# Kernel optimization log

Measured on AMD Instinct MI355X. Metric: run time of the kernel, lower is better.

The kernel has to match this reference:

```python
import jax, jax.numpy as jnp
jax.config.update("jax_enable_x64", True)
import numpy as np

B_, H_, W_, O_ = 8, 96, 96, 8
STRIDES = 1


def generate_px_coordinates(shape, coord_K, strides=1):
    # coord_K: [B,2,2]; row 0 = per-axis scale, row 1 = per-axis offset
    H, W = shape
    u = jnp.arange(W, dtype=coord_K.dtype)[None, None, :]
    v = jnp.arange(H, dtype=coord_K.dtype)[None, :, None]
    u = u * strides * coord_K[:, 0, 0][:, None, None] + coord_K[:, 1, 0][:, None, None]
    v = v * strides * coord_K[:, 0, 1][:, None, None] + coord_K[:, 1, 1][:, None, None]
    B = coord_K.shape[0]
    return jnp.broadcast_to(u, (B, H, W)), jnp.broadcast_to(v, (B, H, W))


def matrix_A(obj, TCR):
    # obj: [B,H,W,O,3]; TCR: [B,4,4] -> A: [B,H,W,O,4,13]
    p1 = obj[..., 0:1]
    p2 = obj[..., 1:2]
    p3 = obj[..., 2:3]
    one = jnp.ones_like(p1)
    T1 = TCR[:, None, None, None, :, 0]
    T2 = TCR[:, None, None, None, :, 1]
    T3 = TCR[:, None, None, None, :, 2]
    T4 = TCR[:, None, None, None, :, 3]
    return jnp.stack((p1 * T1, p2 * T1, p3 * T1,
                      p1 * T2, p2 * T2, p3 * T2,
                      p1 * T3, p2 * T3, p3 * T3,
                      one * T4, one * T1, one * T2, one * T3), axis=-1)


def matrix_B(shape, camera_matrix, coord_K, strides=1):
    # -> [B,H,W,2,4]
    u, v = generate_px_coordinates(shape, coord_K, strides)
    coords = jnp.stack([u, v], axis=-1)[..., None]  # [B,H,W,2,1]
    left4 = -jnp.eye(2, dtype=camera_matrix.dtype)[None, None, None] \
            * camera_matrix[:, None, None, :2, :2]  # [B,H,W,2,2]
    Bn, H, W = u.shape
    left4 = jnp.broadcast_to(left4, (Bn, H, W, 2, 2))
    d1_2 = coords - camera_matrix[:, None, None, :2, 2:3]  # [B,H,W,2,1]
    return jnp.concatenate([left4, d1_2, jnp.zeros_like(d1_2)], axis=-1)


def setup_inputs() -> dict:
    key = jax.random.key(0)
    k1, k2, k3, k4 = jax.random.split(key, 4)
    obj = jax.random.normal(k1, (B_, H_, W_, O_, 3), dtype=jnp.float32)
    w_pixel = jax.random.normal(k2, (B_, H_, W_, O_, 4), dtype=jnp.float32)
    camera_matrix = jax.random.normal(k3, (B_, 3, 3), dtype=jnp.float32)
    coord_K = jax.random.uniform(k4, (B_, 2, 2), dtype=jnp.float32)
    return {"obj": obj, "w_pixel": w_pixel,
            "camera_matrix": camera_matrix, "coord_K": coord_K}


def reference(obj, w_pixel, camera_matrix, coord_K):
    B, H, W, O = obj.shape[:4]
    Wp = w_pixel.reshape(B, H, W, O, 2, 2)
    TCR = jnp.broadcast_to(jnp.eye(4, dtype=obj.dtype), (B, 4, 4))
    A = matrix_A(obj, TCR)                                  # [B,H,W,O,4,13]
    Bm = matrix_B((H, W), camera_matrix, coord_K, STRIDES)  # [B,H,W,2,4]
    BA = jnp.einsum('bxyij,bxyojk->bxyoik', Bm, A)          # [B,H,W,O,2,13]
    MRow = jnp.matmul(Wp, BA)                               # [B,H,W,O,2,13]
    num_eq = 2 * H * W
    M = jnp.transpose(MRow, (0, 3, 1, 2, 4, 5)).reshape(B, O, num_eq, 13)
    M = M.astype(jnp.float64)
    return jnp.matmul(jnp.swapaxes(M, -1, -2), M)           # [B,O,13,13]
```

## Files before the change

### kernel.cpp

```cpp
#include <hip/hip_runtime.h>

#define B_ 8
#define H_ 96
#define W_ 96
#define O_ 8
#define HW_ (H_ * W_)
#define NT 512
#define NPART ((NT / 64) * 8)

__global__ __launch_bounds__(NT) void mtm_kernel(
    const float* __restrict__ obj,
    const float* __restrict__ wpx,
    const float* __restrict__ cam,
    const float* __restrict__ ck,
    float* __restrict__ out)
{
    const int bo = blockIdx.x;
    const int b  = bo >> 3;
    const int o  = bo & 7;

    const float* cm = cam + b * 9;
    const float* k4 = ck  + b * 4;
    const float a   = -cm[0];
    const float c   = -cm[4];
    const float k00 = k4[0];
    const float k01 = k4[1];
    const float Bu  = k4[2] - cm[2];
    const float Bv  = k4[3] - cm[5];

    float acc[60];
#pragma unroll
    for (int s = 0; s < 60; ++s) acc[s] = 0.f;

    const int baseo = (b * HW_) * O_ + o;

    for (int p = threadIdx.x; p < HW_; p += NT) {
        const int h = p / W_;
        const int w = p - h * W_;
        const int slot = baseo + p * O_;

        const float* ob = obj + slot * 3;
        const float p1 = ob[0], p2 = ob[1], p3 = ob[2];
        const float4 wp = *(const float4*)(wpx + slot * 4);

        const float du = fmaf((float)w, k00, Bu);
        const float dv = fmaf((float)h, k01, Bv);

        const float x00 = wp.x * a;
        const float x01 = wp.y * c;
        const float x02 = fmaf(wp.x, du, wp.y * dv);
        const float x10 = wp.z * a;
        const float x11 = wp.w * c;
        const float x12 = fmaf(wp.z, du, wp.w * dv);

        float Xa[6];
        Xa[0] = fmaf(x00, x00, x10 * x10);
        Xa[1] = fmaf(x00, x01, x10 * x11);
        Xa[2] = fmaf(x00, x02, x10 * x12);
        Xa[3] = fmaf(x01, x01, x11 * x11);
        Xa[4] = fmaf(x01, x02, x11 * x12);
        Xa[5] = fmaf(x02, x02, x12 * x12);

        float Q[10];
        Q[0] = p1 * p1; Q[1] = p1 * p2; Q[2] = p1 * p3; Q[3] = p1;
        Q[4] = p2 * p2; Q[5] = p2 * p3; Q[6] = p2;
        Q[7] = p3 * p3; Q[8] = p3;
        Q[9] = 1.f;

#pragma unroll
        for (int ij = 0; ij < 6; ++ij) {
#pragma unroll
            for (int kl = 0; kl < 10; ++kl)
                acc[ij * 10 + kl] = fmaf(Xa[ij], Q[kl], acc[ij * 10 + kl]);
        }
    }

#pragma unroll
    for (int s = 0; s < 60; ++s) {
        float v = acc[s];
        v += __shfl_xor(v, 8,  64);
        v += __shfl_xor(v, 16, 64);
        v += __shfl_xor(v, 32, 64);
        acc[s] = v;
    }

    __shared__ float lds[NPART * 60];
    __shared__ float S[60];
    const int lane = threadIdx.x & 63;
    const int wave = threadIdx.x >> 6;
    if (lane < 8) {
#pragma unroll
        for (int s = 0; s < 60; ++s)
            lds[(wave * 8 + lane) * 60 + s] = acc[s];
    }
    __syncthreads();

    if (threadIdx.x < 60) {
        float v = 0.f;
#pragma unroll
        for (int t = 0; t < NPART; ++t) v += lds[t * 60 + threadIdx.x];
        S[threadIdx.x] = v;
    }
    __syncthreads();

    for (int t = threadIdx.x; t < 169; t += NT) {
        const int r = t / 13;
        const int cc = t - r * 13;
        float val = 0.f;
        if (r != 9 && cc != 9) {
            int i, k, j, l;
            if (r < 9)  { i = r / 3;  k = r - i * 3; } else { i = r - 10;  k = 3; }
            if (cc < 9) { j = cc / 3; l = cc - j * 3; } else { j = cc - 10; l = 3; }
            const int ii = i < j ? i : j, jj = i < j ? j : i;
            const int kk = k < l ? k : l, ll = k < l ? l : k;
            const int ijIdx = ii * (5 - ii) / 2 + jj;
            const int klIdx = kk * (7 - kk) / 2 + ll;
            val = S[ijIdx * 10 + klIdx];
        }
        out[bo * 169 + t] = val;
    }
}

extern "C" void kernel_launch(void* const* d_in, const int* in_sizes, int n_in,
                              void* d_out, int out_size, void* d_ws, size_t ws_size,
                              hipStream_t stream) {
    const float* obj = (const float*)d_in[0];
    const float* wpx = (const float*)d_in[1];
    const float* cam = (const float*)d_in[2];
    const float* ck  = (const float*)d_in[3];
    float* out = (float*)d_out;

    mtm_kernel<<<dim3(B_ * O_), dim3(NT), 0, stream>>>(obj, wpx, cam, ck, out);
}
```

Baseline: 91.07 us.

## Split pixel range across many blocks per batch and reduce via atomics

The grid changes from 64 blocks (one per batch/object pair) to 72 chunks per batch, 576 blocks in all. Within a block, threads map to (object, pixel) so global loads of obj and w_pixel are contiguous. Partial 13x13 results are combined into the output with float atomicAdd after a memset, which aims to fill the GPU instead of leaving most CUs idle. The cost is an extra memset, many atomic adds, and a summation order that now varies from run to run.

Measured after the change: 84.18 us. 7.6% less time.

```diff
diff --git a/kernel.cpp b/kernel.cpp
--- a/kernel.cpp
+++ b/kernel.cpp
@@ -6,7 +6,9 @@
 #define O_ 8
 #define HW_ (H_ * W_)
 #define NT 512
-#define NPART ((NT / 64) * 8)
+#define NCH 72
+#define PPB (HW_ / NCH)
+#define ITERS (PPB / 64)
 
 __global__ __launch_bounds__(NT) void mtm_kernel(
     const float* __restrict__ obj,
@@ -15,9 +17,8 @@
     const float* __restrict__ ck,
     float* __restrict__ out)
 {
-    const int bo = blockIdx.x;
-    const int b  = bo >> 3;
-    const int o  = bo & 7;
+    const int chunk = blockIdx.x;
+    const int b     = blockIdx.y;
 
     const float* cm = cam + b * 9;
     const float* k4 = ck  + b * 4;
@@ -28,20 +29,23 @@
     const float Bu  = k4[2] - cm[2];
     const float Bv  = k4[3] - cm[5];
 
+    const int o  = threadIdx.x & 7;
+    const int pg = threadIdx.x >> 3;
+
     float acc[60];
 #pragma unroll
     for (int s = 0; s < 60; ++s) acc[s] = 0.f;
 
-    const int baseo = (b * HW_) * O_ + o;
-
-    for (int p = threadIdx.x; p < HW_; p += NT) {
+#pragma unroll
+    for (int it = 0; it < ITERS; ++it) {
+        const int p = chunk * PPB + it * 64 + pg;
         const int h = p / W_;
         const int w = p - h * W_;
-        const int slot = baseo + p * O_;
+        const int slot = (b * HW_ + p) * O_ + o;
 
-        const float* ob = obj + slot * 3;
+        const float* ob = obj + (size_t)slot * 3;
         const float p1 = ob[0], p2 = ob[1], p3 = ob[2];
-        const float4 wp = *(const float4*)(wpx + slot * 4);
+        const float4 wp = *(const float4*)(wpx + (size_t)slot * 4);
 
         const float du = fmaf((float)w, k00, Bu);
         const float dv = fmaf((float)h, k01, Bv);
@@ -84,8 +88,8 @@
         acc[s] = v;
     }
 
-    __shared__ float lds[NPART * 60];
-    __shared__ float S[60];
+    __shared__ float lds[64 * 60];
+    __shared__ float Sf[8 * 60];
     const int lane = threadIdx.x & 63;
     const int wave = threadIdx.x >> 6;
     if (lane < 8) {
@@ -95,29 +99,31 @@
     }
     __syncthreads();
 
-    if (threadIdx.x < 60) {
+    if (threadIdx.x < 480) {
+        const int oo = threadIdx.x / 60;
+        const int ss = threadIdx.x - oo * 60;
         float v = 0.f;
 #pragma unroll
-        for (int t = 0; t < NPART; ++t) v += lds[t * 60 + threadIdx.x];
-        S[threadIdx.x] = v;
+        for (int w = 0; w < 8; ++w) v += lds[(w * 8 + oo) * 60 + ss];
+        Sf[oo * 60 + ss] = v;
     }
     __syncthreads();
 
-    for (int t = threadIdx.x; t < 169; t += NT) {
-        const int r = t / 13;
-        const int cc = t - r * 13;
-        float val = 0.f;
-        if (r != 9 && cc != 9) {
-            int i, k, j, l;
-            if (r < 9)  { i = r / 3;  k = r - i * 3; } else { i = r - 10;  k = 3; }
-            if (cc < 9) { j = cc / 3; l = cc - j * 3; } else { j = cc - 10; l = 3; }
-            const int ii = i < j ? i : j, jj = i < j ? j : i;
-            const int kk = k < l ? k : l, ll = k < l ? l : k;
-            const int ijIdx = ii * (5 - ii) / 2 + jj;
-            const int klIdx = kk * (7 - kk) / 2 + ll;
-            val = S[ijIdx * 10 + klIdx];
-        }
-        out[bo * 169 + t] = val;
+    for (int t = threadIdx.x; t < 8 * 169; t += NT) {
+        const int oo = t / 169;
+        const int e  = t - oo * 169;
+        const int r  = e / 13;
+        const int cc = e - r * 13;
+        if (r == 9 || cc == 9) continue;
+        int i, k, j, l;
+        if (r < 9)  { i = r / 3;  k = r - i * 3; } else { i = r - 10;  k = 3; }
+        if (cc < 9) { j = cc / 3; l = cc - j * 3; } else { j = cc - 10; l = 3; }
+        const int ii = i < j ? i : j, jj = i < j ? j : i;
+        const int kk = k < l ? k : l, ll = k < l ? l : k;
+        const int ijIdx = ii * (5 - ii) / 2 + jj;
+        const int klIdx = kk * (7 - kk) / 2 + ll;
+        atomicAdd(out + ((size_t)(b * O_ + oo) * 169 + e),
+                  Sf[oo * 60 + ijIdx * 10 + klIdx]);
     }
 }
 
@@ -130,5 +136,6 @@
     const float* ck  = (const float*)d_in[3];
     float* out = (float*)d_out;
 
-    mtm_kernel<<<dim3(B_ * O_), dim3(NT), 0, stream>>>(obj, wpx, cam, ck, out);
+    hipMemsetAsync(out, 0, (size_t)out_size * sizeof(float), stream);
+    mtm_kernel<<<dim3(NCH, B_), dim3(NT), 0, stream>>>(obj, wpx, cam, ck, out);
 }
```
